# Kernel optimization log

Measured on AMD Instinct MI355X. Metric: run time of the kernel, lower is better.

## Reference

```python
import jax, jax.numpy as jnp
import numpy as np
import math

B, S, D, H = 4, 1024, 512, 8
DK = D // H
NEG = -1e32


def setup_inputs() -> dict:
    key = jax.random.key(0)
    ks = jax.random.split(key, 16)
    f = lambda k, shape: jax.random.normal(k, shape, dtype=jnp.float32)
    w = 1.0 / math.sqrt(D)  # xavier-ish scale
    return {
        'query_mean': f(ks[0], (B, S, D)),
        'query_cov': f(ks[1], (B, S, D)),
        'key_mean': f(ks[2], (B, S, D)),
        'key_cov': f(ks[3], (B, S, D)),
        'values_mean': f(ks[4], (B, S, D)),
        'values_cov': f(ks[5], (B, S, D)),
        'Wk_mean': f(ks[6], (D, D)) * w, 'bk_mean': jnp.zeros((D,), jnp.float32),
        'Wk_cov': f(ks[7], (D, D)) * w, 'bk_cov': jnp.zeros((D,), jnp.float32),
        'Wv_mean': f(ks[8], (D, D)) * w, 'bv_mean': jnp.zeros((D,), jnp.float32),
        'Wv_cov': f(ks[9], (D, D)) * w, 'bv_cov': jnp.zeros((D,), jnp.float32),
        'Wo_mean': f(ks[10], (D, D)) * w, 'bo_mean': jnp.zeros((D,), jnp.float32),
        'Wo_cov': f(ks[11], (D, D)) * w, 'bo_cov': jnp.zeros((D,), jnp.float32),
        'gammas': f(ks[12], (H, 1, 1)) * 0.1,
        'mask': jnp.tril(jnp.ones((1, 1, S, S), dtype=jnp.int32)),
    }


def _forward(query_mean, query_cov, key_mean, key_cov, values_mean, values_cov,
             Wk_mean, bk_mean, Wk_cov, bk_cov, Wv_mean, bv_mean, Wv_cov, bv_cov,
             Wo_mean, bo_mean, Wo_cov, bo_cov, gammas, mask):
    def heads(x, W, b):  # [B,S,D] -> [B,H,S,DK]
        return (x @ W + b).reshape(B, S, H, DK).transpose(0, 2, 1, 3)

    # kq_same=True: queries and keys share the k linears
    qm = heads(query_mean, Wk_mean, bk_mean)
    qc = heads(query_cov, Wk_cov, bk_cov)
    km = heads(key_mean, Wk_mean, bk_mean)
    kc = heads(key_cov, Wk_cov, bk_cov)
    vm = heads(values_mean, Wv_mean, bv_mean)
    vc = heads(values_cov, Wv_cov, bv_cov)

    inv = 1.0 / math.sqrt(DK)
    sm = jnp.einsum('bhqd,bhkd->bhqk', qm, km) * inv  # [B,H,S,S]
    sc = jnp.einsum('bhqd,bhkd->bhqk', qc, kc) * inv

    maskf = mask.astype(jnp.float32)
    # position_effect[i,j] = |j - i|
    pos = jnp.abs(jnp.arange(S)[None, :] - jnp.arange(S)[:, None]).astype(jnp.float32)[None, None]

    def dist_scores(s):
        p = jax.nn.softmax(jnp.where(mask == 0, NEG, s), axis=-1) * maskf
        cum = jnp.cumsum(p, axis=-1)
        tot = jnp.sum(p, axis=-1, keepdims=True)
        return jnp.sqrt(jnp.clip((tot - cum) * pos, 0.0, None))

    dm = jax.lax.stop_gradient(dist_scores(sm))  # torch no_grad + detach
    dc = jax.lax.stop_gradient(dist_scores(sc))

    gv = -jax.nn.softplus(gammas)[None]  # [1,H,1,1]
    em = jnp.clip(jnp.exp(dm * gv), 1e-5, 1e5)
    ec = jnp.clip(jnp.exp(dc * gv), 1e-5, 1e5)

    am = jax.nn.softmax(jnp.where(mask == 0, NEG, sm * em), axis=-1)
    ac = jax.nn.softmax(jnp.where(mask == 0, NEG, sc * ec), axis=-1)

    om = jnp.einsum('bhqk,bhkd->bhqd', am, vm).transpose(0, 2, 1, 3).reshape(B, S, D)
    oc = jnp.einsum('bhqk,bhkd->bhqd', ac, vc).transpose(0, 2, 1, 3).reshape(B, S, D)
    return om @ Wo_mean + bo_mean, oc @ Wo_cov + bo_cov


def reference(query_mean, query_cov, key_mean, key_cov, values_mean, values_cov,
              Wk_mean, bk_mean, Wk_cov, bk_cov, Wv_mean, bv_mean, Wv_cov, bv_cov,
              Wo_mean, bo_mean, Wo_cov, bo_cov, gammas, mask):
    return _forward(query_mean, query_cov, key_mean, key_cov, values_mean, values_cov,
                    Wk_mean, bk_mean, Wk_cov, bk_cov, Wv_mean, bv_mean, Wv_cov, bv_cov,
                    Wo_mean, bo_mean, Wo_cov, bo_cov, gammas, mask)
```

## Files before the change

### kernel.cpp

```cpp
#include <hip/hip_runtime.h>
#include <hip/hip_bf16.h>
#include <math.h>

constexpr int B_  = 4;
constexpr int S_  = 1024;
constexpr int D_  = 512;
constexpr int H_  = 8;
constexpr int DK_ = 64;
constexpr int MROWS_ = B_ * S_;
constexpr size_t SZ_ = (size_t)B_ * H_ * S_ * DK_;
constexpr size_t WSZ_ = (size_t)D_ * D_;

typedef __attribute__((ext_vector_type(8))) short bf16x8;
typedef __attribute__((ext_vector_type(4))) float f32x4;

__device__ __forceinline__ float bf2f(unsigned short u) {
  union { unsigned int u; float f; } v; v.u = (unsigned int)u << 16; return v.f;
}
__device__ __forceinline__ unsigned short f2bf(float f) {
  union { float f; unsigned int u; } v; v.f = f;
  unsigned int r = v.u + 0x7FFFu + ((v.u >> 16) & 1u);
  return (unsigned short)(r >> 16);
}

template <int CTRL>
__device__ __forceinline__ float dpp_mov_f(float x) {
  return __builtin_bit_cast(float,
      __builtin_amdgcn_update_dpp(0, __builtin_bit_cast(int, x), CTRL, 0xF, 0xF, true));
}
__device__ __forceinline__ float scan16(float v) {
  v += dpp_mov_f<0x111>(v);
  v += dpp_mov_f<0x112>(v);
  v += dpp_mov_f<0x114>(v);
  v += dpp_mov_f<0x118>(v);
  return v;
}
__device__ __forceinline__ float red16(float v) {
  v += dpp_mov_f<0x128>(v);
  v += dpp_mov_f<0x124>(v);
  v += dpp_mov_f<0x122>(v);
  v += dpp_mov_f<0x121>(v);
  return v;
}
__device__ __forceinline__ float bcast15(float v) {
  return __builtin_bit_cast(float,
      __builtin_amdgcn_ds_swizzle(__builtin_bit_cast(int, v), 0x01F0));
}

struct TpArgs { const float* W[4]; unsigned short* out[4]; };

__global__ __launch_bounds__(256) void wtrans(TpArgs a) {
  const int z = blockIdx.z;
  const float* __restrict__ W = a.W[z];
  unsigned short* __restrict__ out = a.out[z];
  __shared__ float T[64][65];
  const int tid = threadIdx.x;
  const int tx = blockIdx.x & 7, ty = blockIdx.x >> 3;
  const int k0 = ty * 64, n0 = tx * 64;
#pragma unroll
  for (int i = 0; i < 4; ++i) {
    const int idx = tid + i * 256;
    const int r = idx >> 4, c4 = (idx & 15) * 4;
    const float4 w = *(const float4*)&W[(size_t)(k0 + r) * D_ + n0 + c4];
    T[r][c4 + 0] = w.x; T[r][c4 + 1] = w.y; T[r][c4 + 2] = w.z; T[r][c4 + 3] = w.w;
  }
  __syncthreads();
#pragma unroll
  for (int i = 0; i < 4; ++i) {
    const int idx = tid + i * 256;
    const int n = idx >> 4, kc = (idx & 15) * 4;
    ushort4 pk;
    pk.x = f2bf(T[kc + 0][n]); pk.y = f2bf(T[kc + 1][n]);
    pk.z = f2bf(T[kc + 2][n]); pk.w = f2bf(T[kc + 3][n]);
    *(ushort4*)&out[(size_t)(n0 + n) * D_ + k0 + kc] = pk;
  }
}

struct ProjArgs {
  const float* A[6]; const unsigned short* Wt[6]; const float* bias[6];
  unsigned short* out[6]; int vmode[6];
};

__global__ __launch_bounds__(256) void proj_mfma(ProjArgs args) {
  const int z = blockIdx.z;
  const float* __restrict__ A = args.A[z];
  const unsigned short* __restrict__ Wt = args.Wt[z];
  const float* __restrict__ bias = args.bias[z];
  unsigned short* __restrict__ out = args.out[z];
  const int vmode = args.vmode[z];

  __shared__ unsigned short Abuf[128][40];
  __shared__ unsigned short Bbuf[128][40];
  const int tid = threadIdx.x, wv = tid >> 6, lane = tid & 63;
  const int quad = lane >> 4, l16 = lane & 15;
  const int wm = wv >> 1, wn = wv & 1;
  const int n0 = blockIdx.x * 128, m0 = blockIdx.y * 128;

  f32x4 acc[4][4];
#pragma unroll
  for (int i = 0; i < 4; ++i)
#pragma unroll
    for (int j = 0; j < 4; ++j) acc[i][j] = (f32x4){0.f, 0.f, 0.f, 0.f};

  for (int kt = 0; kt < 16; ++kt) {
    const int k0 = kt * 32;
    __syncthreads();
#pragma unroll
    for (int i = 0; i < 4; ++i) {
      const int idx = tid + i * 256;
      const int m = idx >> 3, c = idx & 7;
      const float4 av = *(const float4*)&A[(size_t)(m0 + m) * D_ + k0 + c * 4];
      ushort4 p;
      p.x = f2bf(av.x); p.y = f2bf(av.y); p.z = f2bf(av.z); p.w = f2bf(av.w);
      *(ushort4*)&Abuf[m][c * 4] = p;
    }
#pragma unroll
    for (int i = 0; i < 2; ++i) {
      const int idx = tid + i * 256;
      const int n = idx >> 2, c = idx & 3;
      *(uint4*)&Bbuf[n][c * 8] = *(const uint4*)&Wt[(size_t)(n0 + n) * D_ + k0 + c * 8];
    }
    __syncthreads();

    bf16x8 af[4], bfr[4];
#pragma unroll
    for (int i = 0; i < 4; ++i) af[i] = *(const bf16x8*)&Abuf[wm * 64 + i * 16 + l16][quad * 8];
#pragma unroll
    for (int j = 0; j < 4; ++j) bfr[j] = *(const bf16x8*)&Bbuf[wn * 64 + j * 16 + l16][quad * 8];
#pragma unroll
    for (int i = 0; i < 4; ++i)
#pragma unroll
      for (int j = 0; j < 4; ++j)
        acc[i][j] = __builtin_amdgcn_mfma_f32_16x16x32_bf16(af[i], bfr[j], acc[i][j], 0, 0, 0);
  }

#pragma unroll
  for (int j = 0; j < 4; ++j) {
    const int col = n0 + wn * 64 + j * 16 + l16;
    const float bv = bias[col];
    const int h = col >> 6, dk = col & 63;
#pragma unroll
    for (int i = 0; i < 4; ++i) {
      const int mbase = m0 + wm * 64 + i * 16 + quad * 4;
      const int b = mbase >> 10;
      if (!vmode) {
#pragma unroll
        for (int r = 0; r < 4; ++r) {
          const int s = (mbase + r) & 1023;
          out[(((size_t)b * H_ + h) * S_ + s) * DK_ + dk] = f2bf(acc[i][j][r] + bv);
        }
      } else {
        const int s = mbase & 1023;
        ushort4 pk;
        pk.x = f2bf(acc[i][j][0] + bv); pk.y = f2bf(acc[i][j][1] + bv);
        pk.z = f2bf(acc[i][j][2] + bv); pk.w = f2bf(acc[i][j][3] + bv);
        *(ushort4*)&out[(((size_t)b * H_ + h) * DK_ + dk) * S_ + s] = pk;
      }
    }
  }
}

struct OutArgs {
  const unsigned short* A[2]; const unsigned short* Wt[2];
  const float* bias[2]; float* out[2];
};

__global__ __launch_bounds__(256) void out_mfma(OutArgs args) {
  const int z = blockIdx.z;
  const unsigned short* __restrict__ A = args.A[z];
  const unsigned short* __restrict__ Wt = args.Wt[z];
  const float* __restrict__ bias = args.bias[z];
  float* __restrict__ out = args.out[z];

  __shared__ unsigned short Abuf[128][40];
  __shared__ unsigned short Bbuf[128][40];
  const int tid = threadIdx.x, wv = tid >> 6, lane = tid & 63;
  const int quad = lane >> 4, l16 = lane & 15;
  const int wm = wv >> 1, wn = wv & 1;
  const int n0 = blockIdx.x * 128, m0 = blockIdx.y * 128;

  f32x4 acc[4][4];
#pragma unroll
  for (int i = 0; i < 4; ++i)
#pragma unroll
    for (int j = 0; j < 4; ++j) acc[i][j] = (f32x4){0.f, 0.f, 0.f, 0.f};

  for (int kt = 0; kt < 16; ++kt) {
    const int k0 = kt * 32;
    __syncthreads();
#pragma unroll
    for (int i = 0; i < 2; ++i) {
      const int idx = tid + i * 256;
      const int m = idx >> 2, c = idx & 3;
      *(uint4*)&Abuf[m][c * 8] = *(const uint4*)&A[(size_t)(m0 + m) * D_ + k0 + c * 8];
    }
#pragma unroll
    for (int i = 0; i < 2; ++i) {
      const int idx = tid + i * 256;
      const int n = idx >> 2, c = idx & 3;
      *(uint4*)&Bbuf[n][c * 8] = *(const uint4*)&Wt[(size_t)(n0 + n) * D_ + k0 + c * 8];
    }
    __syncthreads();

    bf16x8 af[4], bfr[4];
#pragma unroll
    for (int i = 0; i < 4; ++i) af[i] = *(const bf16x8*)&Abuf[wm * 64 + i * 16 + l16][quad * 8];
#pragma unroll
    for (int j = 0; j < 4; ++j) bfr[j] = *(const bf16x8*)&Bbuf[wn * 64 + j * 16 + l16][quad * 8];
#pragma unroll
    for (int i = 0; i < 4; ++i)
#pragma unroll
      for (int j = 0; j < 4; ++j)
        acc[i][j] = __builtin_amdgcn_mfma_f32_16x16x32_bf16(af[i], bfr[j], acc[i][j], 0, 0, 0);
  }

#pragma unroll
  for (int j = 0; j < 4; ++j) {
    const int col = n0 + wn * 64 + j * 16 + l16;
    const float bv = bias[col];
#pragma unroll
    for (int i = 0; i < 4; ++i) {
      const int mbase = m0 + wm * 64 + i * 16 + quad * 4;
#pragma unroll
      for (int r = 0; r < 4; ++r)
        out[(size_t)(mbase + r) * D_ + col] = acc[i][j][r] + bv;
    }
  }
}

__global__ __launch_bounds__(256) void attn_mfma(
    const unsigned short* __restrict__ qkv, const float* __restrict__ gammas,
    unsigned short* __restrict__ Obase)
{
  __shared__ unsigned short Ps[4][16][72];

  const int tid = threadIdx.x;
  const int w = tid >> 6, lane = tid & 63, quad = lane >> 4, l16 = lane & 15;
  const int t  = 63 - blockIdx.y;
  const int bh = (blockIdx.x << 2) + w;
  const int ch = blockIdx.z;
  const int b = bh >> 3, h = bh & 7;
  const int nc = (t >> 2) + 1;
  const int row0 = t << 4;

  const unsigned short* Q  = qkv + (size_t)ch * 3 * SZ_ + (size_t)bh * S_ * DK_;
  const unsigned short* K  = qkv + (size_t)ch * 3 * SZ_ + SZ_ + (size_t)bh * S_ * DK_;
  const unsigned short* Vt = qkv + (size_t)ch * 3 * SZ_ + 2 * SZ_ + (size_t)bh * (size_t)DK_ * S_;
  unsigned short* O = Obase + (size_t)ch * SZ_;

  const float g = gammas[h];
  const float gv = -(fmaxf(g, 0.f) + log1pf(__expf(-fabsf(g))));

  const unsigned short* Qrow = Q + (size_t)(row0 + l16) * DK_;
  const bf16x8 qf0 = *(const bf16x8*)(Qrow + quad * 8);
  const bf16x8 qf1 = *(const bf16x8*)(Qrow + 32 + quad * 8);
  const int myrow = row0 + quad * 4;

  float Tacc[4] = {0.f, 0.f, 0.f, 0.f};
  for (int c = 0; c < nc; ++c) {
    f32x4 sa[4];
#pragma unroll
    for (int cb = 0; cb < 4; ++cb) {
      const unsigned short* Kr = K + (size_t)(c * 64 + cb * 16 + l16) * DK_;
      const bf16x8 kf0 = *(const bf16x8*)(Kr + quad * 8);
      const bf16x8 kf1 = *(const bf16x8*)(Kr + 32 + quad * 8);
      f32x4 a = {0.f, 0.f, 0.f, 0.f};
      a = __builtin_amdgcn_mfma_f32_16x16x32_bf16(qf0, kf0, a, 0, 0, 0);
      a = __builtin_amdgcn_mfma_f32_16x16x32_bf16(qf1, kf1, a, 0, 0, 0);
      sa[cb] = a;
    }
    if (c == nc - 1) {
#pragma unroll
      for (int cb = 0; cb < 4; ++cb)
#pragma unroll
        for (int r = 0; r < 4; ++r) {
          float e = __expf(sa[cb][r] * 0.125f);
          if ((c * 64 + cb * 16 + l16) > (myrow + r)) e = 0.f;
          Tacc[r] += e;
        }
    } else {
#pragma unroll
      for (int cb = 0; cb < 4; ++cb)
#pragma unroll
        for (int r = 0; r < 4; ++r)
          Tacc[r] += __expf(sa[cb][r] * 0.125f);
    }
  }
  float invT[4];
#pragma unroll
  for (int r = 0; r < 4; ++r) invT[r] = 1.f / red16(Tacc[r]);

  float carry[4] = {0.f, 0.f, 0.f, 0.f};
  float l2a[4] = {0.f, 0.f, 0.f, 0.f};
  f32x4 oacc[4];
#pragma unroll
  for (int cb = 0; cb < 4; ++cb) oacc[cb] = (f32x4){0.f, 0.f, 0.f, 0.f};

  for (int c = 0; c < nc; ++c) {
    bf16x8 vf0[4], vf1[4];
#pragma unroll
    for (int cb = 0; cb < 4; ++cb) {
      const unsigned short* Vr = Vt + (size_t)(cb * 16 + l16) * S_ + c * 64;
      vf0[cb] = *(const bf16x8*)(Vr + quad * 8);
      vf1[cb] = *(const bf16x8*)(Vr + 32 + quad * 8);
    }

    f32x4 sa[4];
#pragma unroll
    for (int cb = 0; cb < 4; ++cb) {
      const unsigned short* Kr = K + (size_t)(c * 64 + cb * 16 + l16) * DK_;
      const bf16x8 kf0 = *(const bf16x8*)(Kr + quad * 8);
      const bf16x8 kf1 = *(const bf16x8*)(Kr + 32 + quad * 8);
      f32x4 a = {0.f, 0.f, 0.f, 0.f};
      a = __builtin_amdgcn_mfma_f32_16x16x32_bf16(qf0, kf0, a, 0, 0, 0);
      a = __builtin_amdgcn_mfma_f32_16x16x32_bf16(qf1, kf1, a, 0, 0, 0);
      sa[cb] = a;
    }
#pragma unroll
    for (int cb = 0; cb < 4; ++cb)
#pragma unroll
      for (int r = 0; r < 4; ++r) sa[cb][r] *= 0.125f;
    if (c == nc - 1) {
#pragma unroll
      for (int cb = 0; cb < 4; ++cb)
#pragma unroll
        for (int r = 0; r < 4; ++r)
          if ((c * 64 + cb * 16 + l16) > (myrow + r)) sa[cb][r] = -1e30f;
    }

#pragma unroll
    for (int r = 0; r < 4; ++r) {
      float v0 = scan16(__expf(sa[0][r]));
      float v1 = scan16(__expf(sa[1][r]));
      float v2 = scan16(__expf(sa[2][r]));
      float v3 = scan16(__expf(sa[3][r]));
      const float tt0 = bcast15(v0), tt1 = bcast15(v1);
      const float tt2 = bcast15(v2), tt3 = bcast15(v3);
      const float base = carry[r];
      const float p01 = tt0 + tt1, p012 = p01 + tt2;
      const float cum0 = (base + v0) * invT[r];
      const float cum1 = (base + tt0 + v1) * invT[r];
      const float cum2 = (base + p01 + v2) * invT[r];
      const float cum3 = (base + p012 + v3) * invT[r];
      carry[r] = base + p012 + tt3;

      const float bpos = (float)(myrow + r) - (float)(c * 64 + l16);
      float st0, st1, st2, st3;
      {
        float dd = sqrtf(fmaxf((1.f - cum0) * bpos, 0.f));
        st0 = sa[0][r] * fmaxf(__expf(dd * gv), 1e-5f);
        dd = sqrtf(fmaxf((1.f - cum1) * (bpos - 16.f), 0.f));
        st1 = sa[1][r] * fmaxf(__expf(dd * gv), 1e-5f);
        dd = sqrtf(fmaxf((1.f - cum2) * (bpos - 32.f), 0.f));
        st2 = sa[2][r] * fmaxf(__expf(dd * gv), 1e-5f);
        dd = sqrtf(fmaxf((1.f - cum3) * (bpos - 48.f), 0.f));
        st3 = sa[3][r] * fmaxf(__expf(dd * gv), 1e-5f);
      }

      const float w0 = __expf(st0), w1 = __expf(st1);
      const float w2 = __expf(st2), w3 = __expf(st3);
      l2a[r] += (w0 + w1) + (w2 + w3);
      const int prow = quad * 4 + r;
      Ps[w][prow][ 0 + l16] = f2bf(w0);
      Ps[w][prow][16 + l16] = f2bf(w1);
      Ps[w][prow][32 + l16] = f2bf(w2);
      Ps[w][prow][48 + l16] = f2bf(w3);
    }
    asm volatile("s_waitcnt lgkmcnt(0)" ::: "memory");

    const bf16x8 pf0 = *(const bf16x8*)&Ps[w][l16][quad * 8];
    const bf16x8 pf1 = *(const bf16x8*)&Ps[w][l16][32 + quad * 8];
#pragma unroll
    for (int cb = 0; cb < 4; ++cb) {
      oacc[cb] = __builtin_amdgcn_mfma_f32_16x16x32_bf16(pf0, vf0[cb], oacc[cb], 0, 0, 0);
      oacc[cb] = __builtin_amdgcn_mfma_f32_16x16x32_bf16(pf1, vf1[cb], oacc[cb], 0, 0, 0);
    }
  }

#pragma unroll
  for (int r = 0; r < 4; ++r) {
    const float inv = 1.f / red16(l2a[r]);
    const int srow = myrow + r;
    const size_t base = ((size_t)b * S_ + srow) * D_ + h * DK_;
    O[base +  0 + l16] = f2bf(oacc[0][r] * inv);
    O[base + 16 + l16] = f2bf(oacc[1][r] * inv);
    O[base + 32 + l16] = f2bf(oacc[2][r] * inv);
    O[base + 48 + l16] = f2bf(oacc[3][r] * inv);
  }
}

extern "C" void kernel_launch(void* const* d_in, const int* in_sizes, int n_in,
                              void* d_out, int out_size, void* d_ws, size_t ws_size,
                              hipStream_t stream) {
  const float* query_mean  = (const float*)d_in[0];
  const float* query_cov   = (const float*)d_in[1];
  const float* key_mean    = (const float*)d_in[2];
  const float* key_cov     = (const float*)d_in[3];
  const float* values_mean = (const float*)d_in[4];
  const float* values_cov  = (const float*)d_in[5];
  const float* Wk_mean = (const float*)d_in[6];
  const float* bk_mean = (const float*)d_in[7];
  const float* Wk_cov  = (const float*)d_in[8];
  const float* bk_cov  = (const float*)d_in[9];
  const float* Wv_mean = (const float*)d_in[10];
  const float* bv_mean = (const float*)d_in[11];
  const float* Wv_cov  = (const float*)d_in[12];
  const float* bv_cov  = (const float*)d_in[13];
  const float* Wo_mean = (const float*)d_in[14];
  const float* bo_mean = (const float*)d_in[15];
  const float* Wo_cov  = (const float*)d_in[16];
  const float* bo_cov  = (const float*)d_in[17];
  const float* gammas  = (const float*)d_in[18];

  unsigned short* qkv  = (unsigned short*)d_ws;
  unsigned short* obuf = qkv + 6 * SZ_;
  unsigned short* Wt4  = (unsigned short*)d_out;
  unsigned short* Wot  = qkv + 2 * SZ_;
  float* out = (float*)d_out;

  TpArgs t1;
  t1.W[0] = Wk_mean; t1.W[1] = Wv_mean; t1.W[2] = Wk_cov; t1.W[3] = Wv_cov;
  for (int i = 0; i < 4; ++i) t1.out[i] = Wt4 + (size_t)i * WSZ_;
  wtrans<<<dim3(64, 1, 4), 256, 0, stream>>>(t1);

  ProjArgs pa;
  const float* pA[6] = {query_mean, key_mean, values_mean, query_cov, key_cov, values_cov};
  const int   wIdx[6] = {0, 0, 1, 2, 2, 3};
  const float* pb[6] = {bk_mean, bk_mean, bv_mean, bk_cov, bk_cov, bv_cov};
  const int pv[6] = {0, 0, 1, 0, 0, 1};
  for (int i = 0; i < 6; ++i) {
    pa.A[i] = pA[i]; pa.Wt[i] = Wt4 + (size_t)wIdx[i] * WSZ_; pa.bias[i] = pb[i];
    pa.out[i] = qkv + (size_t)i * SZ_; pa.vmode[i] = pv[i];
  }
  proj_mfma<<<dim3(4, 32, 6), 256, 0, stream>>>(pa);

  attn_mfma<<<dim3(8, 64, 2), 256, 0, stream>>>(qkv, gammas, obuf);

  TpArgs t2;
  t2.W[0] = Wo_mean; t2.W[1] = Wo_cov; t2.W[2] = Wo_mean; t2.W[3] = Wo_cov;
  t2.out[0] = Wot; t2.out[1] = Wot + WSZ_; t2.out[2] = Wot; t2.out[3] = Wot + WSZ_;
  wtrans<<<dim3(64, 1, 2), 256, 0, stream>>>(t2);

  OutArgs oa;
  oa.A[0] = obuf;        oa.A[1] = obuf + SZ_;
  oa.Wt[0] = Wot;        oa.Wt[1] = Wot + WSZ_;
  oa.bias[0] = bo_mean;  oa.bias[1] = bo_cov;
  oa.out[0] = out;       oa.out[1] = out + (size_t)MROWS_ * D_;
  out_mfma<<<dim3(4, 32, 2), 256, 0, stream>>>(oa);
}
```

Measured before the change: 295.4 us.

## Split attention key range across two wave halves and merge via shared memory

The attention kernel now uses 512-thread blocks, each covering one (batch, head) and a 64-row query group. The key chunks are split between two halves of the block. Partial softmax denominators are exchanged through shared memory so the second half can start its cumulative sum from the first half's total. Its output accumulators are then added into the first half's before the store. The aim is to shorten the serial per-wave loop over key chunks and balance the causal workload, at the cost of two block barriers, extra shared memory, and a reduction step.

```diff
diff --git a/kernel.cpp b/kernel.cpp
--- a/kernel.cpp
+++ b/kernel.cpp
@@ -228,28 +228,34 @@
   }
 }
 
-__global__ __launch_bounds__(256) void attn_mfma(
+__global__ __launch_bounds__(512) void attn_mfma(
     const unsigned short* __restrict__ qkv, const float* __restrict__ gammas,
     unsigned short* __restrict__ Obase)
 {
-  __shared__ unsigned short Ps[4][16][72];
+  __shared__ unsigned short Ps[8][16][72];
+  __shared__ float Tpart[2][4][16];
+  __shared__ float Ex[4][64][21];
 
   const int tid = threadIdx.x;
   const int w = tid >> 6, lane = tid & 63, quad = lane >> 4, l16 = lane & 15;
-  const int t  = 63 - blockIdx.y;
-  const int bh = (blockIdx.x << 2) + w;
+  const int g  = 15 - blockIdx.y;
+  const int bh = blockIdx.x;
   const int ch = blockIdx.z;
+  const int sub = w & 3, half = w >> 2;
   const int b = bh >> 3, h = bh & 7;
-  const int nc = (t >> 2) + 1;
-  const int row0 = t << 4;
+  const int nc = g + 1;
+  const int hsplit = (nc + 1) >> 1;
+  const int c_begin = half ? hsplit : 0;
+  const int c_end   = half ? nc : hsplit;
+  const int row0 = g * 64 + sub * 16;
 
   const unsigned short* Q  = qkv + (size_t)ch * 3 * SZ_ + (size_t)bh * S_ * DK_;
   const unsigned short* K  = qkv + (size_t)ch * 3 * SZ_ + SZ_ + (size_t)bh * S_ * DK_;
   const unsigned short* Vt = qkv + (size_t)ch * 3 * SZ_ + 2 * SZ_ + (size_t)bh * (size_t)DK_ * S_;
   unsigned short* O = Obase + (size_t)ch * SZ_;
 
-  const float g = gammas[h];
-  const float gv = -(fmaxf(g, 0.f) + log1pf(__expf(-fabsf(g))));
+  const float g0 = gammas[h];
+  const float gv = -(fmaxf(g0, 0.f) + log1pf(__expf(-fabsf(g0))));
 
   const unsigned short* Qrow = Q + (size_t)(row0 + l16) * DK_;
   const bf16x8 qf0 = *(const bf16x8*)(Qrow + quad * 8);
@@ -257,7 +263,7 @@
   const int myrow = row0 + quad * 4;
 
   float Tacc[4] = {0.f, 0.f, 0.f, 0.f};
-  for (int c = 0; c < nc; ++c) {
+  for (int c = c_begin; c < c_end; ++c) {
     f32x4 sa[4];
 #pragma unroll
     for (int cb = 0; cb < 4; ++cb) {
@@ -269,7 +275,7 @@
       a = __builtin_amdgcn_mfma_f32_16x16x32_bf16(qf1, kf1, a, 0, 0, 0);
       sa[cb] = a;
     }
-    if (c == nc - 1) {
+    if (c == g) {
 #pragma unroll
       for (int cb = 0; cb < 4; ++cb)
 #pragma unroll
@@ -286,17 +292,29 @@
           Tacc[r] += __expf(sa[cb][r] * 0.125f);
     }
   }
-  float invT[4];
-#pragma unroll
-  for (int r = 0; r < 4; ++r) invT[r] = 1.f / red16(Tacc[r]);
-
-  float carry[4] = {0.f, 0.f, 0.f, 0.f};
+#pragma unroll
+  for (int r = 0; r < 4; ++r) Tacc[r] = red16(Tacc[r]);
+  if (l16 == 0) {
+#pragma unroll
+    for (int r = 0; r < 4; ++r) Tpart[half][sub][quad * 4 + r] = Tacc[r];
+  }
+  __syncthreads();
+
+  float invT[4], carry[4];
+#pragma unroll
+  for (int r = 0; r < 4; ++r) {
+    const float tlo = Tpart[0][sub][quad * 4 + r];
+    const float thi = Tpart[1][sub][quad * 4 + r];
+    invT[r] = 1.f / (tlo + thi);
+    carry[r] = half ? tlo : 0.f;
+  }
+
   float l2a[4] = {0.f, 0.f, 0.f, 0.f};
   f32x4 oacc[4];
 #pragma unroll
   for (int cb = 0; cb < 4; ++cb) oacc[cb] = (f32x4){0.f, 0.f, 0.f, 0.f};
 
-  for (int c = 0; c < nc; ++c) {
+  for (int c = c_begin; c < c_end; ++c) {
     bf16x8 vf0[4], vf1[4];
 #pragma unroll
     for (int cb = 0; cb < 4; ++cb) {
@@ -320,7 +338,7 @@
     for (int cb = 0; cb < 4; ++cb)
 #pragma unroll
       for (int r = 0; r < 4; ++r) sa[cb][r] *= 0.125f;
-    if (c == nc - 1) {
+    if (c == g) {
 #pragma unroll
       for (int cb = 0; cb < 4; ++cb)
 #pragma unroll
@@ -377,15 +395,32 @@
     }
   }
 
-#pragma unroll
-  for (int r = 0; r < 4; ++r) {
-    const float inv = 1.f / red16(l2a[r]);
-    const int srow = myrow + r;
-    const size_t base = ((size_t)b * S_ + srow) * D_ + h * DK_;
-    O[base +  0 + l16] = f2bf(oacc[0][r] * inv);
-    O[base + 16 + l16] = f2bf(oacc[1][r] * inv);
-    O[base + 32 + l16] = f2bf(oacc[2][r] * inv);
-    O[base + 48 + l16] = f2bf(oacc[3][r] * inv);
+  if (half) {
+#pragma unroll
+    for (int cb = 0; cb < 4; ++cb)
+#pragma unroll
+      for (int r = 0; r < 4; ++r) Ex[sub][lane][cb * 4 + r] = oacc[cb][r];
+#pragma unroll
+    for (int r = 0; r < 4; ++r) Ex[sub][lane][16 + r] = l2a[r];
+  }
+  __syncthreads();
+  if (!half) {
+#pragma unroll
+    for (int cb = 0; cb < 4; ++cb)
+#pragma unroll
+      for (int r = 0; r < 4; ++r) oacc[cb][r] += Ex[sub][lane][cb * 4 + r];
+#pragma unroll
+    for (int r = 0; r < 4; ++r) l2a[r] += Ex[sub][lane][16 + r];
+#pragma unroll
+    for (int r = 0; r < 4; ++r) {
+      const float inv = 1.f / red16(l2a[r]);
+      const int srow = myrow + r;
+      const size_t base = ((size_t)b * S_ + srow) * D_ + h * DK_;
+      O[base +  0 + l16] = f2bf(oacc[0][r] * inv);
+      O[base + 16 + l16] = f2bf(oacc[1][r] * inv);
+      O[base + 32 + l16] = f2bf(oacc[2][r] * inv);
+      O[base + 48 + l16] = f2bf(oacc[3][r] * inv);
+    }
   }
 }
 
@@ -434,7 +469,7 @@
   }
   proj_mfma<<<dim3(4, 32, 6), 256, 0, stream>>>(pa);
 
-  attn_mfma<<<dim3(8, 64, 2), 256, 0, stream>>>(qkv, gammas, obuf);
+  attn_mfma<<<dim3(32, 16, 2), 512, 0, stream>>>(qkv, gammas, obuf);
 
   TpArgs t2;
   t2.W[0] = Wo_mean; t2.W[1] = Wo_cov; t2.W[2] = Wo_mean; t2.W[3] = Wo_cov;
```

Result: faster. 278.2 us (-5.8%).

## Process 32 query rows per single-wave attention block and fold score scale into Q projection

Applied to the files above, without the earlier changes.

Each attention block becomes one 64-thread wave that handles 32 query rows (two 16-row tiles) for a single batch-head, so every K and V fragment loaded serves two MFMA tiles. The old layout packed four head-waves per block, each doing 16 rows. The 1/sqrt(dk) scale is folded into the Q projection epilogue, which removes the per-score multiply in both attention passes. This halves redundant K/V global loads but doubles per-wave register use, and coarser causal tiles mean more masked work on the diagonal chunk.

```diff
diff --git a/kernel.cpp b/kernel.cpp
--- a/kernel.cpp
+++ b/kernel.cpp
@@ -78,7 +78,7 @@
 
 struct ProjArgs {
   const float* A[6]; const unsigned short* Wt[6]; const float* bias[6];
-  unsigned short* out[6]; int vmode[6];
+  unsigned short* out[6]; int vmode[6]; float scale[6];
 };
 
 __global__ __launch_bounds__(256) void proj_mfma(ProjArgs args) {
@@ -88,6 +88,7 @@
   const float* __restrict__ bias = args.bias[z];
   unsigned short* __restrict__ out = args.out[z];
   const int vmode = args.vmode[z];
+  const float scale = args.scale[z];
 
   __shared__ unsigned short Abuf[128][40];
   __shared__ unsigned short Bbuf[128][40];
@@ -147,7 +148,7 @@
 #pragma unroll
         for (int r = 0; r < 4; ++r) {
           const int s = (mbase + r) & 1023;
-          out[(((size_t)b * H_ + h) * S_ + s) * DK_ + dk] = f2bf(acc[i][j][r] + bv);
+          out[(((size_t)b * H_ + h) * S_ + s) * DK_ + dk] = f2bf((acc[i][j][r] + bv) * scale);
         }
       } else {
         const int s = mbase & 1023;
@@ -228,75 +229,77 @@
   }
 }
 
-__global__ __launch_bounds__(256) void attn_mfma(
+__global__ __launch_bounds__(64) void attn_mfma(
     const unsigned short* __restrict__ qkv, const float* __restrict__ gammas,
     unsigned short* __restrict__ Obase)
 {
-  __shared__ unsigned short Ps[4][16][72];
-
-  const int tid = threadIdx.x;
-  const int w = tid >> 6, lane = tid & 63, quad = lane >> 4, l16 = lane & 15;
-  const int t  = 63 - blockIdx.y;
-  const int bh = (blockIdx.x << 2) + w;
+  __shared__ unsigned short Ps[32][72];
+
+  const int lane = threadIdx.x, quad = lane >> 4, l16 = lane & 15;
+  const int G  = 31 - blockIdx.y;
+  const int bh = blockIdx.x;
   const int ch = blockIdx.z;
   const int b = bh >> 3, h = bh & 7;
-  const int nc = (t >> 2) + 1;
-  const int row0 = t << 4;
+  const int nc = (G >> 1) + 1;
+  const int row0 = G * 32;
 
   const unsigned short* Q  = qkv + (size_t)ch * 3 * SZ_ + (size_t)bh * S_ * DK_;
   const unsigned short* K  = qkv + (size_t)ch * 3 * SZ_ + SZ_ + (size_t)bh * S_ * DK_;
   const unsigned short* Vt = qkv + (size_t)ch * 3 * SZ_ + 2 * SZ_ + (size_t)bh * (size_t)DK_ * S_;
   unsigned short* O = Obase + (size_t)ch * SZ_;
 
-  const float g = gammas[h];
-  const float gv = -(fmaxf(g, 0.f) + log1pf(__expf(-fabsf(g))));
-
-  const unsigned short* Qrow = Q + (size_t)(row0 + l16) * DK_;
-  const bf16x8 qf0 = *(const bf16x8*)(Qrow + quad * 8);
-  const bf16x8 qf1 = *(const bf16x8*)(Qrow + 32 + quad * 8);
-  const int myrow = row0 + quad * 4;
-
-  float Tacc[4] = {0.f, 0.f, 0.f, 0.f};
+  const float g0 = gammas[h];
+  const float gv = -(fmaxf(g0, 0.f) + log1pf(__expf(-fabsf(g0))));
+
+  const unsigned short* Qr0 = Q + (size_t)(row0 + l16) * DK_;
+  const unsigned short* Qr1 = Q + (size_t)(row0 + 16 + l16) * DK_;
+  const bf16x8 qfa0 = *(const bf16x8*)(Qr0 + quad * 8);
+  const bf16x8 qfa1 = *(const bf16x8*)(Qr0 + 32 + quad * 8);
+  const bf16x8 qfb0 = *(const bf16x8*)(Qr1 + quad * 8);
+  const bf16x8 qfb1 = *(const bf16x8*)(Qr1 + 32 + quad * 8);
+  const int myrow0 = row0 + quad * 4;
+  const int myrow1 = row0 + 16 + quad * 4;
+
+  float Ta[2][4] = {{0.f}};
   for (int c = 0; c < nc; ++c) {
-    f32x4 sa[4];
+    const bool last = (c == nc - 1);
 #pragma unroll
     for (int cb = 0; cb < 4; ++cb) {
       const unsigned short* Kr = K + (size_t)(c * 64 + cb * 16 + l16) * DK_;
       const bf16x8 kf0 = *(const bf16x8*)(Kr + quad * 8);
       const bf16x8 kf1 = *(const bf16x8*)(Kr + 32 + quad * 8);
-      f32x4 a = {0.f, 0.f, 0.f, 0.f};
-      a = __builtin_amdgcn_mfma_f32_16x16x32_bf16(qf0, kf0, a, 0, 0, 0);
-      a = __builtin_amdgcn_mfma_f32_16x16x32_bf16(qf1, kf1, a, 0, 0, 0);
-      sa[cb] = a;
-    }
-    if (c == nc - 1) {
-#pragma unroll
-      for (int cb = 0; cb < 4; ++cb)
-#pragma unroll
-        for (int r = 0; r < 4; ++r) {
-          float e = __expf(sa[cb][r] * 0.125f);
-          if ((c * 64 + cb * 16 + l16) > (myrow + r)) e = 0.f;
-          Tacc[r] += e;
-        }
-    } else {
-#pragma unroll
-      for (int cb = 0; cb < 4; ++cb)
-#pragma unroll
-        for (int r = 0; r < 4; ++r)
-          Tacc[r] += __expf(sa[cb][r] * 0.125f);
-    }
-  }
-  float invT[4];
-#pragma unroll
-  for (int r = 0; r < 4; ++r) invT[r] = 1.f / red16(Tacc[r]);
-
-  float carry[4] = {0.f, 0.f, 0.f, 0.f};
-  float l2a[4] = {0.f, 0.f, 0.f, 0.f};
-  f32x4 oacc[4];
-#pragma unroll
-  for (int cb = 0; cb < 4; ++cb) oacc[cb] = (f32x4){0.f, 0.f, 0.f, 0.f};
+      f32x4 s0 = {0.f, 0.f, 0.f, 0.f}, s1 = {0.f, 0.f, 0.f, 0.f};
+      s0 = __builtin_amdgcn_mfma_f32_16x16x32_bf16(qfa0, kf0, s0, 0, 0, 0);
+      s0 = __builtin_amdgcn_mfma_f32_16x16x32_bf16(qfa1, kf1, s0, 0, 0, 0);
+      s1 = __builtin_amdgcn_mfma_f32_16x16x32_bf16(qfb0, kf0, s1, 0, 0, 0);
+      s1 = __builtin_amdgcn_mfma_f32_16x16x32_bf16(qfb1, kf1, s1, 0, 0, 0);
+      const int key = c * 64 + cb * 16 + l16;
+#pragma unroll
+      for (int r = 0; r < 4; ++r) {
+        float e0 = __expf(s0[r]);
+        float e1 = __expf(s1[r]);
+        if (last && key > (myrow0 + r)) e0 = 0.f;
+        if (last && key > (myrow1 + r)) e1 = 0.f;
+        Ta[0][r] += e0; Ta[1][r] += e1;
+      }
+    }
+  }
+  float invT[2][4];
+#pragma unroll
+  for (int t = 0; t < 2; ++t)
+#pragma unroll
+    for (int r = 0; r < 4; ++r) invT[t][r] = 1.f / red16(Ta[t][r]);
+
+  float carry[2][4] = {{0.f}};
+  float l2a[2][4] = {{0.f}};
+  f32x4 oacc[2][4];
+#pragma unroll
+  for (int t = 0; t < 2; ++t)
+#pragma unroll
+    for (int cb = 0; cb < 4; ++cb) oacc[t][cb] = (f32x4){0.f, 0.f, 0.f, 0.f};
 
   for (int c = 0; c < nc; ++c) {
+    const bool last = (c == nc - 1);
     bf16x8 vf0[4], vf1[4];
 #pragma unroll
     for (int cb = 0; cb < 4; ++cb) {
@@ -304,88 +307,101 @@
       vf0[cb] = *(const bf16x8*)(Vr + quad * 8);
       vf1[cb] = *(const bf16x8*)(Vr + 32 + quad * 8);
     }
-
-    f32x4 sa[4];
+    f32x4 sa[2][4];
 #pragma unroll
     for (int cb = 0; cb < 4; ++cb) {
       const unsigned short* Kr = K + (size_t)(c * 64 + cb * 16 + l16) * DK_;
       const bf16x8 kf0 = *(const bf16x8*)(Kr + quad * 8);
       const bf16x8 kf1 = *(const bf16x8*)(Kr + 32 + quad * 8);
-      f32x4 a = {0.f, 0.f, 0.f, 0.f};
-      a = __builtin_amdgcn_mfma_f32_16x16x32_bf16(qf0, kf0, a, 0, 0, 0);
-      a = __builtin_amdgcn_mfma_f32_16x16x32_bf16(qf1, kf1, a, 0, 0, 0);
-      sa[cb] = a;
-    }
-#pragma unroll
-    for (int cb = 0; cb < 4; ++cb)
-#pragma unroll
-      for (int r = 0; r < 4; ++r) sa[cb][r] *= 0.125f;
-    if (c == nc - 1) {
-#pragma unroll
-      for (int cb = 0; cb < 4; ++cb)
-#pragma unroll
-        for (int r = 0; r < 4; ++r)
-          if ((c * 64 + cb * 16 + l16) > (myrow + r)) sa[cb][r] = -1e30f;
-    }
-
+      f32x4 s0 = {0.f, 0.f, 0.f, 0.f}, s1 = {0.f, 0.f, 0.f, 0.f};
+      s0 = __builtin_amdgcn_mfma_f32_16x16x32_bf16(qfa0, kf0, s0, 0, 0, 0);
+      s0 = __builtin_amdgcn_mfma_f32_16x16x32_bf16(qfa1, kf1, s0, 0, 0, 0);
+      s1 = __builtin_amdgcn_mfma_f32_16x16x32_bf16(qfb0, kf0, s1, 0, 0, 0);
+      s1 = __builtin_amdgcn_mfma_f32_16x16x32_bf16(qfb1, kf1, s1, 0, 0, 0);
+      sa[0][cb] = s0; sa[1][cb] = s1;
+    }
+    if (last) {
+#pragma unroll
+      for (int cb = 0; cb < 4; ++cb) {
+        const int key = c * 64 + cb * 16 + l16;
+#pragma unroll
+        for (int r = 0; r < 4; ++r) {
+          if (key > (myrow0 + r)) sa[0][cb][r] = -1e30f;
+          if (key > (myrow1 + r)) sa[1][cb][r] = -1e30f;
+        }
+      }
+    }
+
+#pragma unroll
+    for (int t = 0; t < 2; ++t) {
+      const int rowbase = t ? myrow1 : myrow0;
+#pragma unroll
+      for (int r = 0; r < 4; ++r) {
+        float v0 = scan16(__expf(sa[t][0][r]));
+        float v1 = scan16(__expf(sa[t][1][r]));
+        float v2 = scan16(__expf(sa[t][2][r]));
+        float v3 = scan16(__expf(sa[t][3][r]));
+        const float tt0 = bcast15(v0), tt1 = bcast15(v1);
+        const float tt2 = bcast15(v2), tt3 = bcast15(v3);
+        const float base = carry[t][r];
+        const float p01 = tt0 + tt1, p012 = p01 + tt2;
+        const float iT = invT[t][r];
+        const float cum0 = (base + v0) * iT;
+        const float cum1 = (base + tt0 + v1) * iT;
+        const float cum2 = (base + p01 + v2) * iT;
+        const float cum3 = (base + p012 + v3) * iT;
+        carry[t][r] = base + p012 + tt3;
+
+        const float bpos = (float)(rowbase + r) - (float)(c * 64 + l16);
+        float st0, st1, st2, st3;
+        {
+          float dd = sqrtf(fmaxf((1.f - cum0) * bpos, 0.f));
+          st0 = sa[t][0][r] * fmaxf(__expf(dd * gv), 1e-5f);
+          dd = sqrtf(fmaxf((1.f - cum1) * (bpos - 16.f), 0.f));
+          st1 = sa[t][1][r] * fmaxf(__expf(dd * gv), 1e-5f);
+          dd = sqrtf(fmaxf((1.f - cum2) * (bpos - 32.f), 0.f));
+          st2 = sa[t][2][r] * fmaxf(__expf(dd * gv), 1e-5f);
+          dd = sqrtf(fmaxf((1.f - cum3) * (bpos - 48.f), 0.f));
+          st3 = sa[t][3][r] * fmaxf(__expf(dd * gv), 1e-5f);
+        }
+
+        const float w0 = __expf(st0), w1 = __expf(st1);
+        const float w2 = __expf(st2), w3 = __expf(st3);
+        l2a[t][r] += (w0 + w1) + (w2 + w3);
+        const int prow = t * 16 + quad * 4 + r;
+        Ps[prow][ 0 + l16] = f2bf(w0);
+        Ps[prow][16 + l16] = f2bf(w1);
+        Ps[prow][32 + l16] = f2bf(w2);
+        Ps[prow][48 + l16] = f2bf(w3);
+      }
+    }
+    asm volatile("s_waitcnt lgkmcnt(0)" ::: "memory");
+
+    const bf16x8 pfa0 = *(const bf16x8*)&Ps[l16][quad * 8];
+    const bf16x8 pfa1 = *(const bf16x8*)&Ps[l16][32 + quad * 8];
+    const bf16x8 pfb0 = *(const bf16x8*)&Ps[16 + l16][quad * 8];
+    const bf16x8 pfb1 = *(const bf16x8*)&Ps[16 + l16][32 + quad * 8];
+#pragma unroll
+    for (int cb = 0; cb < 4; ++cb) {
+      oacc[0][cb] = __builtin_amdgcn_mfma_f32_16x16x32_bf16(pfa0, vf0[cb], oacc[0][cb], 0, 0, 0);
+      oacc[0][cb] = __builtin_amdgcn_mfma_f32_16x16x32_bf16(pfa1, vf1[cb], oacc[0][cb], 0, 0, 0);
+      oacc[1][cb] = __builtin_amdgcn_mfma_f32_16x16x32_bf16(pfb0, vf0[cb], oacc[1][cb], 0, 0, 0);
+      oacc[1][cb] = __builtin_amdgcn_mfma_f32_16x16x32_bf16(pfb1, vf1[cb], oacc[1][cb], 0, 0, 0);
+    }
+  }
+
+#pragma unroll
+  for (int t = 0; t < 2; ++t) {
+    const int rowbase = t ? myrow1 : myrow0;
 #pragma unroll
     for (int r = 0; r < 4; ++r) {
-      float v0 = scan16(__expf(sa[0][r]));
-      float v1 = scan16(__expf(sa[1][r]));
-      float v2 = scan16(__expf(sa[2][r]));
-      float v3 = scan16(__expf(sa[3][r]));
-      const float tt0 = bcast15(v0), tt1 = bcast15(v1);
-      const float tt2 = bcast15(v2), tt3 = bcast15(v3);
-      const float base = carry[r];
-      const float p01 = tt0 + tt1, p012 = p01 + tt2;
-      const float cum0 = (base + v0) * invT[r];
-      const float cum1 = (base + tt0 + v1) * invT[r];
-      const float cum2 = (base + p01 + v2) * invT[r];
-      const float cum3 = (base + p012 + v3) * invT[r];
-      carry[r] = base + p012 + tt3;
-
-      const float bpos = (float)(myrow + r) - (float)(c * 64 + l16);
-      float st0, st1, st2, st3;
-      {
-        float dd = sqrtf(fmaxf((1.f - cum0) * bpos, 0.f));
-        st0 = sa[0][r] * fmaxf(__expf(dd * gv), 1e-5f);
-        dd = sqrtf(fmaxf((1.f - cum1) * (bpos - 16.f), 0.f));
-        st1 = sa[1][r] * fmaxf(__expf(dd * gv), 1e-5f);
-        dd = sqrtf(fmaxf((1.f - cum2) * (bpos - 32.f), 0.f));
-        st2 = sa[2][r] * fmaxf(__expf(dd * gv), 1e-5f);
-        dd = sqrtf(fmaxf((1.f - cum3) * (bpos - 48.f), 0.f));
-        st3 = sa[3][r] * fmaxf(__expf(dd * gv), 1e-5f);
-      }
-
-      const float w0 = __expf(st0), w1 = __expf(st1);
-      const float w2 = __expf(st2), w3 = __expf(st3);
-      l2a[r] += (w0 + w1) + (w2 + w3);
-      const int prow = quad * 4 + r;
-      Ps[w][prow][ 0 + l16] = f2bf(w0);
-      Ps[w][prow][16 + l16] = f2bf(w1);
-      Ps[w][prow][32 + l16] = f2bf(w2);
-      Ps[w][prow][48 + l16] = f2bf(w3);
-    }
-    asm volatile("s_waitcnt lgkmcnt(0)" ::: "memory");
-
-    const bf16x8 pf0 = *(const bf16x8*)&Ps[w][l16][quad * 8];
-    const bf16x8 pf1 = *(const bf16x8*)&Ps[w][l16][32 + quad * 8];
-#pragma unroll
-    for (int cb = 0; cb < 4; ++cb) {
-      oacc[cb] = __builtin_amdgcn_mfma_f32_16x16x32_bf16(pf0, vf0[cb], oacc[cb], 0, 0, 0);
-      oacc[cb] = __builtin_amdgcn_mfma_f32_16x16x32_bf16(pf1, vf1[cb], oacc[cb], 0, 0, 0);
-    }
-  }
-
-#pragma unroll
-  for (int r = 0; r < 4; ++r) {
-    const float inv = 1.f / red16(l2a[r]);
-    const int srow = myrow + r;
-    const size_t base = ((size_t)b * S_ + srow) * D_ + h * DK_;
-    O[base +  0 + l16] = f2bf(oacc[0][r] * inv);
-    O[base + 16 + l16] = f2bf(oacc[1][r] * inv);
-    O[base + 32 + l16] = f2bf(oacc[2][r] * inv);
-    O[base + 48 + l16] = f2bf(oacc[3][r] * inv);
+      const float inv = 1.f / red16(l2a[t][r]);
+      const size_t base = ((size_t)b * S_ + rowbase + r) * D_ + h * DK_;
+      O[base +  0 + l16] = f2bf(oacc[t][0][r] * inv);
+      O[base + 16 + l16] = f2bf(oacc[t][1][r] * inv);
+      O[base + 32 + l16] = f2bf(oacc[t][2][r] * inv);
+      O[base + 48 + l16] = f2bf(oacc[t][3][r] * inv);
+    }
   }
 }
 
@@ -428,13 +444,14 @@
   const int   wIdx[6] = {0, 0, 1, 2, 2, 3};
   const float* pb[6] = {bk_mean, bk_mean, bv_mean, bk_cov, bk_cov, bv_cov};
   const int pv[6] = {0, 0, 1, 0, 0, 1};
+  const float ps[6] = {0.125f, 1.f, 1.f, 0.125f, 1.f, 1.f};
   for (int i = 0; i < 6; ++i) {
     pa.A[i] = pA[i]; pa.Wt[i] = Wt4 + (size_t)wIdx[i] * WSZ_; pa.bias[i] = pb[i];
-    pa.out[i] = qkv + (size_t)i * SZ_; pa.vmode[i] = pv[i];
+    pa.out[i] = qkv + (size_t)i * SZ_; pa.vmode[i] = pv[i]; pa.scale[i] = ps[i];
   }
   proj_mfma<<<dim3(4, 32, 6), 256, 0, stream>>>(pa);
 
-  attn_mfma<<<dim3(8, 64, 2), 256, 0, stream>>>(qkv, gammas, obuf);
+  attn_mfma<<<dim3(32, 32, 2), 64, 0, stream>>>(qkv, gammas, obuf);
 
   TpArgs t2;
   t2.W[0] = Wo_mean; t2.W[1] = Wo_cov; t2.W[2] = Wo_mean; t2.W[3] = Wo_cov;
```

New measurement: 310.3 us. 5.0% more time.
